# Kernel tuning notes

Measured on AMD Instinct MI355X. Metric: run time of the kernel, lower is better.

## Reference

```python
import jax, jax.numpy as jnp
import numpy as np

N, IN_DIM, OUT_DIM, HEADS, E = 50000, 256, 256, 4, 800000
HEAD_DIM = OUT_DIM // HEADS
NEG_SLOPE = 0.2


def setup_inputs() -> dict:
    key = jax.random.key(0)
    k = jax.random.split(key, 6)
    h = jax.random.normal(k[0], (N, IN_DIM), dtype=jnp.float32)
    edge_index = jax.random.randint(k[1], (2, E), 0, N, dtype=jnp.int32)
    # xavier-uniform-ish scales
    W = jax.random.normal(k[2], (OUT_DIM, IN_DIM), dtype=jnp.float32) * (1.0 / np.sqrt(IN_DIM))
    b = jnp.zeros((OUT_DIM,), dtype=jnp.float32)
    a_src = jax.random.normal(k[3], (HEADS, HEAD_DIM), dtype=jnp.float32) * (1.0 / np.sqrt(HEAD_DIM))
    a_dst = jax.random.normal(k[4], (HEADS, HEAD_DIM), dtype=jnp.float32) * (1.0 / np.sqrt(HEAD_DIM))
    return {"h": h, "edge_index": edge_index, "W": W, "b": b, "a_src": a_src, "a_dst": a_dst}


def reference(h, edge_index, W, b, a_src, a_dst):
    idx_i, idx_j = edge_index[0], edge_index[1]
    Wh = (h @ W.T + b).reshape(N, HEADS, HEAD_DIM)  # [N,H,D]
    # per-node attention logits components (avoids gathering full Wh per edge twice)
    alpha_src = jnp.einsum('nhd,hd->nh', Wh, a_src)  # [N,H]
    alpha_dst = jnp.einsum('nhd,hd->nh', Wh, a_dst)  # [N,H]
    e = jax.nn.leaky_relu(alpha_src[idx_i] + alpha_dst[idx_j], NEG_SLOPE)  # [E,H]
    # segment softmax over neighbors j of each destination row i (sparse.softmax dim=1)
    m = jax.ops.segment_max(e, idx_i, num_segments=N)  # [N,H]
    ex = jnp.exp(e - m[idx_i])
    denom = jax.ops.segment_sum(ex, idx_i, num_segments=N)  # [N,H]
    att = ex / denom[idx_i]  # [E,H]
    # sparse-mm aggregation: out_i = sum_j att_ij * Wh_j, per head
    out = jax.ops.segment_sum(att[:, :, None] * Wh[idx_j], idx_i, num_segments=N)  # [N,H,D]
    return out.reshape(N, OUT_DIM)
```

## Files before the change

### kernel.cpp

```cpp
#include <hip/hip_runtime.h>
#include <hip/hip_bf16.h>
#include <stdint.h>

constexpr int IN_DIM  = 256;
constexpr int OUT_DIM = 256;
constexpr int HEADS   = 4;
constexpr int HEAD_DIM = 64;
constexpr float NEG_SLOPE = 0.2f;

typedef __attribute__((ext_vector_type(8))) short bf16x8;
typedef __attribute__((ext_vector_type(4))) float f32x4;

static __device__ __forceinline__ unsigned short f2bf(float f) {
  union { float f; uint32_t u; } v; v.f = f;
  uint32_t u = v.u;
  return (unsigned short)((u + 0x7fffu + ((u >> 16) & 1u)) >> 16);
}

__global__ __launch_bounds__(256) void k_prep(
    const float* __restrict__ W, const float* __restrict__ b,
    const float* __restrict__ a_src, const float* __restrict__ a_dst,
    float* __restrict__ csrc, unsigned short* __restrict__ Wb,
    int* __restrict__ counts, int N) {
  int bid = blockIdx.x, t = threadIdx.x;
  int i = bid * 256 + t;
  if (i < N) counts[i] = 0;
  if (bid < 32) {
    int base = bid * 2048 + t * 8;
    float4 f0 = *(const float4*)(W + base);
    float4 f1 = *(const float4*)(W + base + 4);
    union { unsigned short us[8]; uint4 u4; } pk;
    pk.us[0]=f2bf(f0.x); pk.us[1]=f2bf(f0.y); pk.us[2]=f2bf(f0.z); pk.us[3]=f2bf(f0.w);
    pk.us[4]=f2bf(f1.x); pk.us[5]=f2bf(f1.y); pk.us[6]=f2bf(f1.z); pk.us[7]=f2bf(f1.w);
    *(uint4*)(Wb + base) = pk.u4;
  } else if (bid == 32 && t < 8) {
    int hh = t & 3;
    const float* a = (t < 4 ? a_src : a_dst) + hh * HEAD_DIM;
    float cs = 0.f;
    for (int d = 0; d < HEAD_DIM; ++d) cs += b[hh * HEAD_DIM + d] * a[d];
    csrc[t] = cs;
  }
}

__global__ __launch_bounds__(256) void k_gemm_mfma(
    const float* __restrict__ h, const unsigned short* __restrict__ Wb,
    const float* __restrict__ b,
    const float* __restrict__ a_src, const float* __restrict__ a_dst,
    const float* __restrict__ csrc,
    unsigned short* __restrict__ Wh,
    float* __restrict__ asrc, float* __restrict__ adst, int N) {
  __shared__ unsigned short lds[20480];
  const int t = threadIdx.x;
  const int w = t >> 6, l = t & 63;
  const int lm = l & 15, g = l >> 4;
  const int r0 = blockIdx.x * 64;

  const int arow = t >> 2;
  {
  }
  int growA = r0 + arow; if (growA > N - 1) growA = N - 1;
  const float* aptr = h + (size_t)growA * 256;

  f32x4 acc[4][4];
  const f32x4 fz = {0.f, 0.f, 0.f, 0.f};
#pragma unroll
  for (int fm = 0; fm < 4; ++fm)
#pragma unroll
    for (int fn = 0; fn < 4; ++fn) acc[fm][fn] = fz;

  float breg[4], asg[4], adg[4];
#pragma unroll
  for (int fn = 0; fn < 4; ++fn) {
    breg[fn] = b[w * 64 + fn * 16 + lm];
    asg[fn]  = a_src[w * 64 + fn * 16 + lm];
    adg[fn]  = a_dst[w * 64 + fn * 16 + lm];
  }

  f32x4 apre[4];

  auto loadA = [&](int ch) {
    int k0 = ch * 64;
#pragma unroll
    for (int cc = 0; cc < 2; ++cc) {
      int c = (t & 3) * 2 + cc;
      apre[cc * 2 + 0] = *(const f32x4*)(aptr + k0 + c * 8);
      apre[cc * 2 + 1] = *(const f32x4*)(aptr + k0 + c * 8 + 4);
    }
  };

  auto writeA = [&]() {
    unsigned short* dstbase = lds + arow * 64;
#pragma unroll
    for (int cc = 0; cc < 2; ++cc) {
      int c = (t & 3) * 2 + cc;
      union { unsigned short us[8]; bf16x8 v; } pk;
      f32x4 f0 = apre[cc * 2 + 0], f1 = apre[cc * 2 + 1];
      pk.us[0]=f2bf(f0.x); pk.us[1]=f2bf(f0.y); pk.us[2]=f2bf(f0.z); pk.us[3]=f2bf(f0.w);
      pk.us[4]=f2bf(f1.x); pk.us[5]=f2bf(f1.y); pk.us[6]=f2bf(f1.z); pk.us[7]=f2bf(f1.w);
      *(bf16x8*)(dstbase + ((c ^ (arow & 7)) * 8)) = pk.v;
    }
  };

  auto stageB = [&](int ch) {
    int k0 = ch * 64;
    unsigned short* Bbase = lds + 4096;
    int c  = l & 7;
    int rs = l >> 3;
#pragma unroll
    for (int i = 0; i < 8; ++i) {
      int row = w * 64 + i * 8 + rs;
      bf16x8 v = *(const bf16x8*)(Wb + (size_t)row * 256 + k0 + c * 8);
      *(bf16x8*)(Bbase + row * 64 + ((c ^ rs) * 8)) = v;
    }
  };

  auto compute = [&]() {
    const unsigned short* A = lds;
    const unsigned short* B = lds + 4096;
#pragma unroll
    for (int ks = 0; ks < 2; ++ks) {
      bf16x8 af[4], bfr[4];
#pragma unroll
      for (int fm = 0; fm < 4; ++fm) {
        int row = fm * 16 + lm;
        af[fm] = *(const bf16x8*)(A + row * 64 + (((ks * 4 + g) ^ (row & 7)) * 8));
      }
#pragma unroll
      for (int fn = 0; fn < 4; ++fn) {
        int row = w * 64 + fn * 16 + lm;
        bfr[fn] = *(const bf16x8*)(B + row * 64 + (((ks * 4 + g) ^ (row & 7)) * 8));
      }
#pragma unroll
      for (int fm = 0; fm < 4; ++fm)
#pragma unroll
        for (int fn = 0; fn < 4; ++fn)
          acc[fm][fn] = __builtin_amdgcn_mfma_f32_16x16x32_bf16(
              af[fm], bfr[fn], acc[fm][fn], 0, 0, 0);
    }
  };

  loadA(0); writeA(); stageB(0);
  __syncthreads();
#pragma unroll
  for (int ch = 0; ch < 4; ++ch) {
    if (ch < 3) loadA(ch + 1);
    compute();
    __syncthreads();
    if (ch < 3) {
      writeA();
      stageB(ch + 1);
      __syncthreads();
    }
  }

#pragma unroll
  for (int fm = 0; fm < 4; ++fm) {
#pragma unroll
    for (int r = 0; r < 4; ++r) {
      int grow = r0 + fm * 16 + g * 4 + r;
      if (grow < N) {
        size_t rowoff = (size_t)grow * 256;
#pragma unroll
        for (int fn = 0; fn < 4; ++fn) {
          int col = w * 64 + fn * 16 + lm;
          Wh[rowoff + col] = f2bf(acc[fm][fn][r] + breg[fn]);
        }
      }
    }
  }

  float cs = csrc[w], cd = csrc[4 + w];
#pragma unroll
  for (int fm = 0; fm < 4; ++fm) {
#pragma unroll
    for (int r = 0; r < 4; ++r) {
      float ps = acc[fm][0][r] * asg[0] + acc[fm][1][r] * asg[1]
               + acc[fm][2][r] * asg[2] + acc[fm][3][r] * asg[3];
      float pd = acc[fm][0][r] * adg[0] + acc[fm][1][r] * adg[1]
               + acc[fm][2][r] * adg[2] + acc[fm][3][r] * adg[3];
#pragma unroll
      for (int off = 1; off < 16; off <<= 1) {
        ps += __shfl_xor(ps, off, 64);
        pd += __shfl_xor(pd, off, 64);
      }
      if (lm == 0) {
        int grow = r0 + fm * 16 + g * 4 + r;
        if (grow < N) {
          asrc[grow * 4 + w] = ps + cs;
          adst[grow * 4 + w] = pd + cd;
        }
      }
    }
  }
}

__global__ __launch_bounds__(256) void k_hist(const int* __restrict__ idx_i,
                                              int* __restrict__ counts, int E) {
  int e = blockIdx.x * 256 + threadIdx.x;
  if (e < E) atomicAdd(&counts[idx_i[e]], 1);
}

__global__ __launch_bounds__(256) void k_scanA(const int* __restrict__ counts,
                                               int* __restrict__ offsets,
                                               int* __restrict__ bsum, int N) {
  __shared__ int s[256];
  int t = threadIdx.x;
  int base = blockIdx.x * 1024 + t * 4;
  int v[4], sum = 0;
#pragma unroll
  for (int k = 0; k < 4; ++k) {
    v[k] = (base + k < N) ? counts[base + k] : 0;
    sum += v[k];
  }
  s[t] = sum;
  __syncthreads();
  for (int off = 1; off < 256; off <<= 1) {
    int x = (t >= off) ? s[t - off] : 0;
    __syncthreads();
    s[t] += x;
    __syncthreads();
  }
  int pre = s[t] - sum;
#pragma unroll
  for (int k = 0; k < 4; ++k) {
    if (base + k < N) offsets[base + k] = pre;
    pre += v[k];
  }
  if (t == 255) bsum[blockIdx.x] = s[255];
}

__global__ __launch_bounds__(256) void k_scanBC(int* __restrict__ offsets,
                                                const int* __restrict__ bsum,
                                                int nb, int N) {
  __shared__ int s[256];
  int t = threadIdx.x;
  int v = (t < nb) ? bsum[t] : 0;
  s[t] = v;
  __syncthreads();
  for (int off = 1; off < 256; off <<= 1) {
    int x = (t >= off) ? s[t - off] : 0;
    __syncthreads();
    s[t] += x;
    __syncthreads();
  }
  int bid = blockIdx.x;
  int add = (bid > 0) ? s[bid - 1] : 0;
  int base = bid * 1024 + t * 4;
#pragma unroll
  for (int k = 0; k < 4; ++k)
    if (base + k < N) offsets[base + k] += add;
}

__global__ __launch_bounds__(256) void k_scatter(const int* __restrict__ idx_i,
                                                 const int* __restrict__ idx_j,
                                                 int* __restrict__ offsets,
                                                 int* __restrict__ csr_j, int E) {
  int e = blockIdx.x * 256 + threadIdx.x;
  if (e < E) {
    int i = idx_i[e];
    int p = atomicAdd(&offsets[i], 1);
    csr_j[p] = idx_j[e];
  }
}

__global__ __launch_bounds__(256) void k_aggregate(const int* __restrict__ offsets,
                                                   const int* __restrict__ csr_j,
                                                   const float* __restrict__ asrc,
                                                   const float* __restrict__ adst,
                                                   const unsigned short* __restrict__ Wh,
                                                   float* __restrict__ out, int N) {
  int t = threadIdx.x;
  int wv = t >> 6, l = t & 63;
  int half = l >> 5, ll = l & 31;
  int i = blockIdx.x * 8 + wv * 2 + half;
  bool valid = i < N;
  int beg = (valid && i > 0) ? offsets[i - 1] : 0;
  int end = valid ? offsets[i] : 0;
  int deg = end - beg;
  int hh = ll >> 3;
  float aih = valid ? asrc[i * 4 + hh] : 0.f;

  float o[8];
#pragma unroll
  for (int d = 0; d < 8; ++d) o[d] = 0.f;
  float denom = 0.f;

  for (int q = 0; q < deg; q += 8) {
    int jj[8];
    float wgt[8];
    uint4 vv[8];
#pragma unroll
    for (int k = 0; k < 8; ++k) {
      int qk = q + k;
      int qc = qk < deg - 1 ? qk : deg - 1;
      jj[k] = csr_j[beg + qc];
    }
#pragma unroll
    for (int k = 0; k < 8; ++k) {
      float s = aih + adst[(size_t)jj[k] * 4 + hh];
      s = s > 0.f ? s : NEG_SLOPE * s;
      s = (q + k < deg) ? s : -1e38f;
      wgt[k] = __expf(s);
      vv[k] = *(const uint4*)(Wh + (size_t)jj[k] * 256 + ll * 8);
    }
    denom += ((wgt[0] + wgt[1]) + (wgt[2] + wgt[3])) +
             ((wgt[4] + wgt[5]) + (wgt[6] + wgt[7]));
#pragma unroll
    for (int k = 0; k < 8; ++k) {
      union { uint32_t u; float f; } c0, c1, c2, c3, c4, c5, c6, c7;
      c0.u = vv[k].x << 16; c1.u = vv[k].x & 0xffff0000u;
      c2.u = vv[k].y << 16; c3.u = vv[k].y & 0xffff0000u;
      c4.u = vv[k].z << 16; c5.u = vv[k].z & 0xffff0000u;
      c6.u = vv[k].w << 16; c7.u = vv[k].w & 0xffff0000u;
      float wk = wgt[k];
      o[0] += wk * c0.f; o[1] += wk * c1.f;
      o[2] += wk * c2.f; o[3] += wk * c3.f;
      o[4] += wk * c4.f; o[5] += wk * c5.f;
      o[6] += wk * c6.f; o[7] += wk * c7.f;
    }
  }

  if (valid) {
    float inv = (deg > 0) ? 1.f / denom : 0.f;
    f32x4 o0 = {o[0] * inv, o[1] * inv, o[2] * inv, o[3] * inv};
    f32x4 o1 = {o[4] * inv, o[5] * inv, o[6] * inv, o[7] * inv};
    f32x4* dst = (f32x4*)(out + (size_t)i * 256 + ll * 8);
    __builtin_nontemporal_store(o0, dst);
    __builtin_nontemporal_store(o1, dst + 1);
  }
}

extern "C" void kernel_launch(void* const* d_in, const int* in_sizes, int n_in,
                              void* d_out, int out_size, void* d_ws, size_t ws_size,
                              hipStream_t stream) {
  const float* h     = (const float*)d_in[0];
  const int*   eidx  = (const int*)  d_in[1];
  const float* W     = (const float*)d_in[2];
  const float* b     = (const float*)d_in[3];
  const float* a_src = (const float*)d_in[4];
  const float* a_dst = (const float*)d_in[5];
  float* out = (float*)d_out;

  const int N = in_sizes[0] / IN_DIM;
  const int E = in_sizes[1] / 2;
  const int* idx_i = eidx;
  const int* idx_j = eidx + E;

  char* p = (char*)d_ws;
  auto alloc = [&](size_t bytes) {
    char* r = p;
    p += (bytes + 255) & ~(size_t)255;
    return r;
  };
  float* csrc = (float*)alloc(8 * sizeof(float));
  unsigned short* Wb = (unsigned short*)alloc((size_t)OUT_DIM * IN_DIM * sizeof(unsigned short));
  unsigned short* Wh = (unsigned short*)alloc((size_t)N * OUT_DIM * sizeof(unsigned short));
  float* asrc = (float*)alloc((size_t)N * HEADS * sizeof(float));
  float* adst = (float*)alloc((size_t)N * HEADS * sizeof(float));
  int* counts  = (int*)alloc((size_t)N * sizeof(int));
  int* offsets = (int*)alloc(((size_t)N + 1) * sizeof(int));
  int* bsum    = (int*)alloc(256 * sizeof(int));
  int* csrj    = (int*)alloc((size_t)E * sizeof(int));

  const int nbN = (N + 255) / 256;
  const int nbE = (E + 255) / 256;
  const int nbM = (N + 63) / 64;
  const int nbS = (N + 1023) / 1024;

  k_prep<<<nbN, 256, 0, stream>>>(W, b, a_src, a_dst, csrc, Wb, counts, N);
  k_gemm_mfma<<<nbM, 256, 0, stream>>>(h, Wb, b, a_src, a_dst, csrc,
                                       Wh, asrc, adst, N);
  k_hist<<<nbE, 256, 0, stream>>>(idx_i, counts, E);
  k_scanA<<<nbS, 256, 0, stream>>>(counts, offsets, bsum, N);
  k_scanBC<<<nbS, 256, 0, stream>>>(offsets, bsum, nbS, N);
  k_scatter<<<nbE, 256, 0, stream>>>(idx_i, idx_j, offsets, csrj, E);
  k_aggregate<<<(N + 7) / 8, 256, 0, stream>>>(offsets, csrj, asrc, adst, Wh, out, N);
}
```

Before: 206.1 us.

## Fuse histogram into GEMM and merge scan+scatter into one cooperative kernel

```diff
diff --git a/kernel.cpp b/kernel.cpp
--- a/kernel.cpp
+++ b/kernel.cpp
@@ -1,6 +1,9 @@
 #include <hip/hip_runtime.h>
 #include <hip/hip_bf16.h>
+#include <hip/hip_cooperative_groups.h>
 #include <stdint.h>
+
+namespace cg = cooperative_groups;
 
 constexpr int IN_DIM  = 256;
 constexpr int OUT_DIM = 256;
@@ -48,7 +51,8 @@
     const float* __restrict__ a_src, const float* __restrict__ a_dst,
     const float* __restrict__ csrc,
     unsigned short* __restrict__ Wh,
-    float* __restrict__ asrc, float* __restrict__ adst, int N) {
+    float* __restrict__ asrc, float* __restrict__ adst,
+    const int* __restrict__ idx_i, int* __restrict__ counts, int N, int E) {
   __shared__ unsigned short lds[20480];
   const int t = threadIdx.x;
   const int w = t >> 6, l = t & 63;
@@ -56,8 +60,6 @@
   const int r0 = blockIdx.x * 64;
 
   const int arow = t >> 2;
-  {
-  }
   int growA = r0 + arow; if (growA > N - 1) growA = N - 1;
   const float* aptr = h + (size_t)growA * 256;
 
@@ -192,71 +194,71 @@
       }
     }
   }
-}
-
-__global__ __launch_bounds__(256) void k_hist(const int* __restrict__ idx_i,
-                                              int* __restrict__ counts, int E) {
-  int e = blockIdx.x * 256 + threadIdx.x;
-  if (e < E) atomicAdd(&counts[idx_i[e]], 1);
-}
-
-__global__ __launch_bounds__(256) void k_scanA(const int* __restrict__ counts,
-                                               int* __restrict__ offsets,
-                                               int* __restrict__ bsum, int N) {
+
+  {
+    long long nb = gridDim.x;
+    long long e0 = (long long)blockIdx.x * E / nb;
+    long long e1 = ((long long)blockIdx.x + 1) * E / nb;
+    for (long long e = e0 + t; e < e1; e += 256)
+      atomicAdd(&counts[idx_i[e]], 1);
+  }
+}
+
+__global__ __launch_bounds__(256) void k_csr(
+    const int* __restrict__ idx_i, const int* __restrict__ idx_j,
+    const int* __restrict__ counts, int* __restrict__ offsets,
+    int* __restrict__ bsum, int* __restrict__ csr_j, int N, int E) {
+  cg::grid_group grid = cg::this_grid();
+  const int t = threadIdx.x, bid = blockIdx.x;
+  const int nthreads = gridDim.x * 256;
+  const int nchunk = (N + 1023) >> 10;
   __shared__ int s[256];
-  int t = threadIdx.x;
-  int base = blockIdx.x * 1024 + t * 4;
-  int v[4], sum = 0;
-#pragma unroll
-  for (int k = 0; k < 4; ++k) {
-    v[k] = (base + k < N) ? counts[base + k] : 0;
-    sum += v[k];
-  }
-  s[t] = sum;
-  __syncthreads();
-  for (int off = 1; off < 256; off <<= 1) {
-    int x = (t >= off) ? s[t - off] : 0;
+
+  if (bid < nchunk) {
+    int base = bid * 1024 + t * 4;
+    int v[4], sum = 0;
+#pragma unroll
+    for (int k = 0; k < 4; ++k) {
+      v[k] = (base + k < N) ? counts[base + k] : 0;
+      sum += v[k];
+    }
+    s[t] = sum;
     __syncthreads();
-    s[t] += x;
+    for (int off = 1; off < 256; off <<= 1) {
+      int x = (t >= off) ? s[t - off] : 0;
+      __syncthreads();
+      s[t] += x;
+      __syncthreads();
+    }
+    int pre = s[t] - sum;
+#pragma unroll
+    for (int k = 0; k < 4; ++k) {
+      if (base + k < N) offsets[base + k] = pre;
+      pre += v[k];
+    }
+    if (t == 255) bsum[bid] = s[255];
+  }
+  grid.sync();
+
+  if (bid < nchunk) {
+    int v2 = (t < nchunk) ? bsum[t] : 0;
+    s[t] = v2;
     __syncthreads();
-  }
-  int pre = s[t] - sum;
-#pragma unroll
-  for (int k = 0; k < 4; ++k) {
-    if (base + k < N) offsets[base + k] = pre;
-    pre += v[k];
-  }
-  if (t == 255) bsum[blockIdx.x] = s[255];
-}
-
-__global__ __launch_bounds__(256) void k_scanBC(int* __restrict__ offsets,
-                                                const int* __restrict__ bsum,
-                                                int nb, int N) {
-  __shared__ int s[256];
-  int t = threadIdx.x;
-  int v = (t < nb) ? bsum[t] : 0;
-  s[t] = v;
-  __syncthreads();
-  for (int off = 1; off < 256; off <<= 1) {
-    int x = (t >= off) ? s[t - off] : 0;
-    __syncthreads();
-    s[t] += x;
-    __syncthreads();
-  }
-  int bid = blockIdx.x;
-  int add = (bid > 0) ? s[bid - 1] : 0;
-  int base = bid * 1024 + t * 4;
-#pragma unroll
-  for (int k = 0; k < 4; ++k)
-    if (base + k < N) offsets[base + k] += add;
-}
-
-__global__ __launch_bounds__(256) void k_scatter(const int* __restrict__ idx_i,
-                                                 const int* __restrict__ idx_j,
-                                                 int* __restrict__ offsets,
-                                                 int* __restrict__ csr_j, int E) {
-  int e = blockIdx.x * 256 + threadIdx.x;
-  if (e < E) {
+    for (int off = 1; off < 256; off <<= 1) {
+      int x = (t >= off) ? s[t - off] : 0;
+      __syncthreads();
+      s[t] += x;
+      __syncthreads();
+    }
+    int add = (bid > 0) ? s[bid - 1] : 0;
+    int base = bid * 1024 + t * 4;
+#pragma unroll
+    for (int k = 0; k < 4; ++k)
+      if (base + k < N) offsets[base + k] += add;
+  }
+  grid.sync();
+
+  for (int e = bid * 256 + t; e < E; e += nthreads) {
     int i = idx_i[e];
     int p = atomicAdd(&offsets[i], 1);
     csr_j[p] = idx_j[e];
@@ -363,16 +365,17 @@
   int* csrj    = (int*)alloc((size_t)E * sizeof(int));
 
   const int nbN = (N + 255) / 256;
-  const int nbE = (E + 255) / 256;
   const int nbM = (N + 63) / 64;
-  const int nbS = (N + 1023) / 1024;
 
   k_prep<<<nbN, 256, 0, stream>>>(W, b, a_src, a_dst, csrc, Wb, counts, N);
   k_gemm_mfma<<<nbM, 256, 0, stream>>>(h, Wb, b, a_src, a_dst, csrc,
-                                       Wh, asrc, adst, N);
-  k_hist<<<nbE, 256, 0, stream>>>(idx_i, counts, E);
-  k_scanA<<<nbS, 256, 0, stream>>>(counts, offsets, bsum, N);
-  k_scanBC<<<nbS, 256, 0, stream>>>(offsets, bsum, nbS, N);
-  k_scatter<<<nbE, 256, 0, stream>>>(idx_i, idx_j, offsets, csrj, E);
+                                       Wh, asrc, adst, idx_i, counts, N, E);
+  {
+    int Nv = N, Ev = E;
+    void* args[] = {(void*)&idx_i, (void*)&idx_j, (void*)&counts, (void*)&offsets,
+                    (void*)&bsum, (void*)&csrj, (void*)&Nv, (void*)&Ev};
+    (void)hipLaunchCooperativeKernel((void*)k_csr, dim3(1024), dim3(256),
+                                     args, 0, stream);
+  }
   k_aggregate<<<(N + 7) / 8, 256, 0, stream>>>(offsets, csrj, asrc, adst, Wh, out, N);
 }
```

After: 426.2 us. +106.8%, slower.
